# Performance work log

Measured on AMD Instinct MI355X. Metric: run time of the kernel, lower is better.

Reference implementation:

```python
import jax, jax.numpy as jnp
import numpy as np

B = 128        # graphs
N_PER = 1024   # nodes per graph
K = 7          # knn neighbors
X_SIZE = 16
POS_SIZE = 3
H1, H2 = 64, 128
N = B * N_PER
EPS = 1e-5


def _lin_init(key, din, dout):
    kw, kb = jax.random.split(key)
    s = 1.0 / np.sqrt(din)
    w = jax.random.uniform(kw, (din, dout), jnp.float32, -s, s)
    b = jax.random.uniform(kb, (dout,), jnp.float32, -s, s)
    return w, b


def setup_inputs() -> dict:
    key = jax.random.key(0)
    ks = jax.random.split(key, 12)
    x = jax.random.normal(ks[0], (N, X_SIZE), jnp.float32)
    pos = jax.random.normal(ks[1], (N, POS_SIZE), jnp.float32)
    batch = jnp.repeat(jnp.arange(B, dtype=jnp.int32), N_PER)
    wk1, bk1 = _lin_init(ks[2], X_SIZE, H1)
    wq1, bq1 = _lin_init(ks[3], X_SIZE, H1)
    wv1, bv1 = _lin_init(ks[4], X_SIZE, H1)
    ws1, bs1 = _lin_init(ks[5], X_SIZE, H1)
    wk2, bk2 = _lin_init(ks[6], H1, H2)
    wq2, bq2 = _lin_init(ks[7], H1, H2)
    wv2, bv2 = _lin_init(ks[8], H1, H2)
    ws2, bs2 = _lin_init(ks[9], H1, H2)
    g1 = jnp.ones((H1,), jnp.float32); be1 = jnp.zeros((H1,), jnp.float32)
    g2 = jnp.ones((H2,), jnp.float32); be2 = jnp.zeros((H2,), jnp.float32)
    return dict(x=x, pos=pos, batch=batch,
                wk1=wk1, bk1=bk1, wq1=wq1, bq1=bq1, wv1=wv1, bv1=bv1, ws1=ws1, bs1=bs1, g1=g1, be1=be1,
                wk2=wk2, bk2=bk2, wq2=wq2, bq2=bq2, wv2=wv2, bv2=bv2, ws2=ws2, bs2=bs2, g2=g2, be2=be2)


def knn_edges(pos):
    # batch-aware kNN: graphs are equal-sized contiguous blocks of N_PER nodes
    p = pos.reshape(B, N_PER, POS_SIZE)
    def per_graph(pg):
        d = jnp.sum((pg[:, None, :] - pg[None, :, :]) ** 2, axis=-1)  # [n, n]
        d = jnp.where(jnp.eye(N_PER, dtype=bool), jnp.inf, d)          # no self loops
        _, idx = jax.lax.top_k(-d, K)                                   # [n, K]
        return idx
    idx = jax.vmap(per_graph)(p)                       # [B, N_PER, K]
    offs = (jnp.arange(B) * N_PER)[:, None, None]
    src = (idx + offs).reshape(-1)                     # neighbor j (source)
    dst = jnp.broadcast_to(jnp.arange(N_PER)[None, :, None] + offs, (B, N_PER, K)).reshape(-1)
    return src, dst


def res_gated_conv(x, src, dst, wk, bk, wq, bq, wv, bv, ws, bs):
    # out_i = skip(x_i) + sum_{j->i} sigmoid(K x_i + Q x_j) * V x_j
    kf = x @ wk + bk
    qf = x @ wq + bq
    vf = x @ wv + bv
    msg = jax.nn.sigmoid(kf[dst] + qf[src]) * vf[src]  # [E, out]
    agg = jnp.zeros_like(kf).at[dst].add(msg)
    return agg + x @ ws + bs


def batch_norm(x, gamma, beta):
    m = x.mean(0)
    v = jnp.mean((x - m) ** 2, 0)  # biased var (training-mode BN)
    return (x - m) * jax.lax.rsqrt(v + EPS) * gamma + beta


def reference(x, pos, batch, wk1, bk1, wq1, bq1, wv1, bv1, ws1, bs1, g1, be1,
              wk2, bk2, wq2, bq2, wv2, bv2, ws2, bs2, g2, be2):
    src, dst = knn_edges(pos)
    h = jax.nn.relu(batch_norm(res_gated_conv(x, src, dst, wk1, bk1, wq1, bq1, wv1, bv1, ws1, bs1), g1, be1))
    h = jax.nn.relu(batch_norm(res_gated_conv(h, src, dst, wk2, bk2, wq2, bq2, wv2, bv2, ws2, bs2), g2, be2))
    s = jax.ops.segment_sum(h, batch, num_segments=B)
    cnt = jax.ops.segment_sum(jnp.ones((h.shape[0], 1), h.dtype), batch, num_segments=B)
    return s / cnt
```

## Files before the change

kernel.cpp:

```cpp
#include <hip/hip_runtime.h>
#include <hip/hip_bf16.h>

#define BGR   128
#define NPER  1024
#define NK    7
#define NNODES (BGR*NPER)

typedef __attribute__((ext_vector_type(8))) short short8;
typedef __attribute__((ext_vector_type(8))) unsigned short ushort8;
typedef __attribute__((ext_vector_type(4))) float floatx4;

static __device__ __forceinline__ float bf2f(unsigned short u) {
    unsigned int x = ((unsigned int)u) << 16;
    return __builtin_bit_cast(float, x);
}
static __device__ __forceinline__ unsigned short f2bf(float f) {
    unsigned int x = __builtin_bit_cast(unsigned int, f);
    unsigned int lsb = (x >> 16) & 1u;
    x += 0x7fffu + lsb;
    return (unsigned short)(x >> 16);
}
static __device__ __forceinline__ float packdi(float d, int j) {
    unsigned int ub = (__builtin_bit_cast(unsigned int, d) & 0xFFFFFC00u) | (unsigned int)j;
    return __builtin_bit_cast(float, ub);
}

__global__ __launch_bounds__(256) void knn_kernel(const float* __restrict__ pos,
                                                  int* __restrict__ idx) {
    __shared__ __align__(16) floatx4 sp[8 * 129];
    int g     = blockIdx.x >> 4;
    int qbase = (blockIdx.x & 15) << 6;
    int base  = g * NPER;
    const float* pg = pos + (size_t)base * 3;
    for (int t = threadIdx.x; t < NPER * 3; t += 256) {
        float v = pg[t];
        int j = t / 3, comp = t - j * 3;
        int slot = (j >> 7) * 129 + (j & 127);
        ((float*)&sp[slot])[comp] = v;
    }
    __syncthreads();
    for (int j = threadIdx.x; j < NPER; j += 256) {
        int slot = (j >> 7) * 129 + (j & 127);
        floatx4 q = sp[slot];
        sp[slot].w = fmaf(q.x, q.x, fmaf(q.y, q.y, q.z * q.z));
    }
    __syncthreads();

    int lane = threadIdx.x & 63;
    int wv   = (int)threadIdx.x >> 6;
    int grp  = lane >> 3;
    int e    = lane & 7;
    int qA_l = qbase + (wv * 8 + grp) * 2;
    int qB_l = qA_l + 1;
    floatx4 meA = sp[(qA_l >> 7) * 129 + (qA_l & 127)];
    floatx4 meB = sp[(qB_l >> 7) * 129 + (qB_l & 127)];
    float mAx = -2.f * meA.x, mAy = -2.f * meA.y, mAz = -2.f * meA.z;
    float mBx = -2.f * meB.x, mBy = -2.f * meB.y, mBz = -2.f * meB.z;
    const floatx4* cp = sp + e * 129;
    int jbase = e << 7;

    float a0=3e38f,a1=3e38f,a2=3e38f,a3=3e38f,a4=3e38f,a5=3e38f,a6=3e38f,a7=3e38f;
    float c0=3e38f,c1=3e38f,c2=3e38f,c3=3e38f,c4=3e38f,c5=3e38f,c6=3e38f,c7=3e38f;
    for (int jp = 0; jp < 128; jp += 4) {
        #pragma unroll
        for (int u = 0; u < 4; ++u) {
            floatx4 q = cp[jp + u];
            float dA = fmaf(mAx, q.x, fmaf(mAy, q.y, fmaf(mAz, q.z, q.w)));
            float dB = fmaf(mBx, q.x, fmaf(mBy, q.y, fmaf(mBz, q.z, q.w)));
            float tA = packdi(dA, jbase + jp + u);
            float tB = packdi(dB, jbase + jp + u);
            float nA7 = __builtin_amdgcn_fmed3f(a6, a7, tA);
            float nA6 = __builtin_amdgcn_fmed3f(a5, a6, tA);
            float nA5 = __builtin_amdgcn_fmed3f(a4, a5, tA);
            float nA4 = __builtin_amdgcn_fmed3f(a3, a4, tA);
            float nA3 = __builtin_amdgcn_fmed3f(a2, a3, tA);
            float nA2 = __builtin_amdgcn_fmed3f(a1, a2, tA);
            float nA1 = __builtin_amdgcn_fmed3f(a0, a1, tA);
            a0 = fminf(a0, tA);
            a1 = nA1; a2 = nA2; a3 = nA3; a4 = nA4; a5 = nA5; a6 = nA6; a7 = nA7;
            float nB7 = __builtin_amdgcn_fmed3f(c6, c7, tB);
            float nB6 = __builtin_amdgcn_fmed3f(c5, c6, tB);
            float nB5 = __builtin_amdgcn_fmed3f(c4, c5, tB);
            float nB4 = __builtin_amdgcn_fmed3f(c3, c4, tB);
            float nB3 = __builtin_amdgcn_fmed3f(c2, c3, tB);
            float nB2 = __builtin_amdgcn_fmed3f(c1, c2, tB);
            float nB1 = __builtin_amdgcn_fmed3f(c0, c1, tB);
            c0 = fminf(c0, tB);
            c1 = nB1; c2 = nB2; c3 = nB3; c4 = nB4; c5 = nB5; c6 = nB6; c7 = nB7;
        }
    }

    float A[8] = {a0,a1,a2,a3,a4,a5,a6,a7};
    float C[8] = {c0,c1,c2,c3,c4,c5,c6,c7};
    #pragma unroll
    for (int st = 0; st < 2; ++st) {
        int mask = 1 << st;
        #pragma unroll
        for (int ch = 0; ch < 2; ++ch) {
            float* L = ch ? C : A;
            float B[8], T[8];
            #pragma unroll
            for (int i = 0; i < 8; ++i) B[i] = __shfl_xor(L[i], mask);
            #pragma unroll
            for (int i = 0; i < 8; ++i) T[i] = fminf(L[i], B[7 - i]);
            #define CEx(x,y) { float mn = fminf(T[x], T[y]); float mx = fmaxf(T[x], T[y]); T[x] = mn; T[y] = mx; }
            CEx(0,4) CEx(1,5) CEx(2,6) CEx(3,7)
            CEx(0,2) CEx(1,3) CEx(4,6) CEx(5,7)
            CEx(0,1) CEx(2,3) CEx(4,5) CEx(6,7)
            #undef CEx
            #pragma unroll
            for (int i = 0; i < 8; ++i) L[i] = T[i];
        }
    }
    float OA[8], OC[8];
    #pragma unroll
    for (int i = 0; i < 8; ++i) { OA[i] = __shfl_xor(A[i], 4); OC[i] = __shfl_xor(C[i], 4); }

    if (e < 2) {
        float *M, *O;
        int qm_l;
        if (e == 0) { M = A;  O = OA; qm_l = qA_l; }
        else        { M = C;  O = OC; qm_l = qB_l; }
        bool selfInM = (qm_l >> 9) == 0;
        int r[7];
        #pragma unroll
        for (int i = 0; i < 7; ++i) {
            float mm = selfInM ? fminf(M[i + 1], O[6 - i]) : fminf(O[i + 1], M[6 - i]);
            r[i] = base + (int)(__builtin_bit_cast(unsigned int, mm) & 1023u);
        }
        int4* op = (int4*)(idx + (size_t)(base + qm_l) * 8);
        int4 r0, r1;
        r0.x = r[0]; r0.y = r[1]; r0.z = r[2]; r0.w = r[3];
        r1.x = r[4]; r1.y = r[5]; r1.z = r[6]; r1.w = base;
        op[0] = r0;
        op[1] = r1;
    }
}

__global__ __launch_bounds__(256) void feat1_kernel(
    const float* __restrict__ x,
    const float* __restrict__ wk, const float* __restrict__ bk,
    const float* __restrict__ wq, const float* __restrict__ bq,
    const float* __restrict__ wv, const float* __restrict__ bv,
    const float* __restrict__ wsm, const float* __restrict__ bs,
    unsigned int* __restrict__ qv, unsigned int* __restrict__ ks) {
    int c = threadIdx.x & 63;
    float Wk[16], Wq[16], Wv[16], Ws[16];
    #pragma unroll
    for (int k = 0; k < 16; ++k) {
        Wk[k] = wk[k*64+c]; Wq[k] = wq[k*64+c]; Wv[k] = wv[k*64+c]; Ws[k] = wsm[k*64+c];
    }
    float Bk = bk[c], Bq = bq[c], Bv = bv[c], Bs = bs[c];
    int wave = blockIdx.x * (blockDim.x >> 6) + (threadIdx.x >> 6);
    int nw   = gridDim.x * (blockDim.x >> 6);
    for (int n = wave; n < NNODES; n += nw) {
        const float* xr = x + (size_t)n * 16;
        float ak = Bk, aq = Bq, av = Bv, as = Bs;
        #pragma unroll
        for (int k = 0; k < 16; ++k) {
            float xv = xr[k];
            ak += xv * Wk[k]; aq += xv * Wq[k]; av += xv * Wv[k]; as += xv * Ws[k];
        }
        size_t o = (size_t)n * 64 + c;
        qv[o] = ((unsigned int)f2bf(av) << 16) | f2bf(aq);
        ks[o] = ((unsigned int)f2bf(as) << 16) | f2bf(ak);
    }
}

template<int C>
__global__ __launch_bounds__(256) void conv_kernel(
    const unsigned int* __restrict__ qv, const unsigned int* __restrict__ ks,
    const int* __restrict__ idx, unsigned short* __restrict__ h,
    float* __restrict__ part) {
    const int NPB = 256 / C;
    int c   = threadIdx.x & (C - 1);
    int sub = __builtin_amdgcn_readfirstlane((int)(threadIdx.x / C));
    int b     = blockIdx.x;
    int xcd   = b & 7;
    int chunk = b >> 3;
    int graph = xcd * 16 + (chunk >> 5);
    int nblk  = chunk & 31;
    int n0 = graph * NPER + nblk * 32;
    float s = 0.f, s2 = 0.f;
    #pragma unroll 4
    for (int i = sub; i < 32; i += NPB) {
        int n = n0 + i;
        const int4* nb4 = (const int4*)(idx + (size_t)n * 8);
        int4 na = nb4[0];
        int4 nbv = nb4[1];
        unsigned int ku = ks[(size_t)n * C + c];
        float kv  = bf2f((unsigned short)(ku & 0xFFFF));
        float acc = bf2f((unsigned short)(ku >> 16));
        int jj[7] = {na.x, na.y, na.z, na.w, nbv.x, nbv.y, nbv.z};
        #pragma unroll
        for (int k = 0; k < NK; ++k) {
            int j = __builtin_amdgcn_readfirstlane(jj[k]);
            const unsigned int* p = qv + (size_t)j * C;
            unsigned int u = p[c];
            float qvv = bf2f((unsigned short)(u & 0xFFFF));
            float vvv = bf2f((unsigned short)(u >> 16));
            float t = kv + qvv;
            float sg = __builtin_amdgcn_rcpf(1.f + __expf(-t));
            acc = fmaf(sg, vvv, acc);
        }
        unsigned short hb = f2bf(acc);
        h[(size_t)n * C + c] = hb;
        float hv = bf2f(hb);
        s += hv; s2 += hv * hv;
    }
    __shared__ float ls[256], ls2[256];
    ls[threadIdx.x] = s; ls2[threadIdx.x] = s2;
    __syncthreads();
    if (threadIdx.x < C) {
        #pragma unroll
        for (int l = 1; l < NPB; ++l) { s += ls[threadIdx.x + l*C]; s2 += ls2[threadIdx.x + l*C]; }
        part[(size_t)blockIdx.x * 2 * C + threadIdx.x]     = s;
        part[(size_t)blockIdx.x * 2 * C + C + threadIdx.x] = s2;
    }
}

template<int C>
static __device__ __forceinline__ void bnfin_body(
    const float* __restrict__ part, const float* __restrict__ gamma,
    const float* __restrict__ beta, float* __restrict__ ss,
    int c, float* ls, float* ls2) {
    float s = 0.f, s2 = 0.f;
    for (int b = threadIdx.x; b < 4096; b += 256) {
        s  += part[(size_t)b * 2 * C + c];
        s2 += part[(size_t)b * 2 * C + C + c];
    }
    ls[threadIdx.x] = s; ls2[threadIdx.x] = s2;
    __syncthreads();
    for (int st = 128; st > 0; st >>= 1) {
        if (threadIdx.x < st) { ls[threadIdx.x] += ls[threadIdx.x+st]; ls2[threadIdx.x] += ls2[threadIdx.x+st]; }
        __syncthreads();
    }
    if (threadIdx.x == 0) {
        float m   = ls[0] / (float)NNODES;
        float var = ls2[0] / (float)NNODES - m * m;
        float inv = rsqrtf(var + 1e-5f);
        float sc  = gamma[c] * inv;
        ss[c]     = sc;
        ss[C + c] = beta[c] - m * sc;
    }
}

template<int C>
__global__ __launch_bounds__(256) void bnfin_kernel(
    const float* __restrict__ part, const float* __restrict__ gamma,
    const float* __restrict__ beta, float* __restrict__ ss) {
    __shared__ float ls[256], ls2[256];
    bnfin_body<C>(part, gamma, beta, ss, blockIdx.x, ls, ls2);
}

__global__ __launch_bounds__(256) void fin1_wfrag_kernel(
    const float* __restrict__ part, const float* __restrict__ gamma,
    const float* __restrict__ beta, float* __restrict__ ss,
    const float* __restrict__ w0, const float* __restrict__ w1,
    const float* __restrict__ w2, const float* __restrict__ w3,
    unsigned short* __restrict__ frag) {
    __shared__ float ls[256], ls2[256];
    if (blockIdx.x < 64) {
        bnfin_body<64>(part, gamma, beta, ss, blockIdx.x, ls, ls2);
        return;
    }
    int s  = blockIdx.x - 64;
    if (threadIdx.x >= 64) return;
    int m  = s >> 4;
    int kt = (s >> 3) & 1;
    int ct = s & 7;
    const float* w = (m == 0) ? w0 : (m == 1) ? w1 : (m == 2) ? w2 : w3;
    int l = threadIdx.x;
    int col = ct * 16 + (l & 15);
    int kbase = kt * 32 + (l >> 4) * 8;
    unsigned short* out = frag + ((size_t)s * 64 + l) * 8;
    #pragma unroll
    for (int e = 0; e < 8; ++e) out[e] = f2bf(w[(size_t)(kbase + e) * 128 + col]);
}

__global__ __launch_bounds__(256) void feat2_kernel(
    const unsigned short* __restrict__ h1n, const unsigned short* __restrict__ frag,
    const float* __restrict__ ss1,
    const float* __restrict__ b0, const float* __restrict__ b1,
    const float* __restrict__ b2, const float* __restrict__ b3,
    unsigned int* __restrict__ qv2, unsigned int* __restrict__ ks2) {
    __shared__ unsigned short xh[2][2][16][17];
    int m  = threadIdx.x >> 6;
    int l  = threadIdx.x & 63;
    const float* bm = (m == 0) ? b0 : (m == 1) ? b1 : (m == 2) ? b2 : b3;
    int lr = l & 15;
    int gq = l >> 4;
    short8 W0[8], W1[8];
    #pragma unroll
    for (int ct = 0; ct < 8; ++ct) {
        W0[ct] = *(const short8*)(frag + ((size_t)(m * 16 + ct)     * 64 + l) * 8);
        W1[ct] = *(const short8*)(frag + ((size_t)(m * 16 + 8 + ct) * 64 + l) * 8);
    }
    float bvv[8];
    #pragma unroll
    for (int ct = 0; ct < 8; ++ct) bvv[ct] = bm[ct * 16 + lr];

    for (int t = 0; t < 8; ++t) {
        int nt = blockIdx.x * 8 + t;
        int n  = nt * 16 + lr;
        const unsigned short* ar = h1n + (size_t)n * 64 + gq * 8;
        short8 a0r = *(const short8*)ar;
        short8 a1r = *(const short8*)(ar + 32);
        short8 a0, a1;
        #pragma unroll
        for (int e = 0; e < 8; ++e) {
            int c0 = gq * 8 + e;
            float f0 = bf2f((unsigned short)a0r[e]) * ss1[c0] + ss1[64 + c0];
            a0[e] = (short)f2bf(fmaxf(f0, 0.f));
            int c1 = 32 + gq * 8 + e;
            float f1 = bf2f((unsigned short)a1r[e]) * ss1[c1] + ss1[64 + c1];
            a1[e] = (short)f2bf(fmaxf(f1, 0.f));
        }
        #pragma unroll
        for (int ct = 0; ct < 8; ++ct) {
            float bv = bvv[ct];
            floatx4 acc = {bv, bv, bv, bv};
            acc = __builtin_amdgcn_mfma_f32_16x16x32_bf16(a0, W0[ct], acc, 0, 0, 0);
            acc = __builtin_amdgcn_mfma_f32_16x16x32_bf16(a1, W1[ct], acc, 0, 0, 0);
            if (m >= 2) {
                #pragma unroll
                for (int r = 0; r < 4; ++r)
                    xh[ct & 1][m - 2][gq * 4 + r][lr] = f2bf(acc[r]);
            }
            __syncthreads();
            if (m < 2) {
                unsigned int* od = (m == 1) ? qv2 : ks2;
                int set = (m == 1) ? 0 : 1;
                #pragma unroll
                for (int r = 0; r < 4; ++r) {
                    unsigned int lo = f2bf(acc[r]);
                    unsigned int hi = xh[ct & 1][set][gq * 4 + r][lr];
                    od[(size_t)(nt * 16 + gq * 4 + r) * 128 + ct * 16 + lr] = (hi << 16) | lo;
                }
            }
        }
    }
}

__global__ __launch_bounds__(256) void pool_partial_kernel(const unsigned int* __restrict__ h2p,
                                                           const float* __restrict__ ss2,
                                                           float* __restrict__ part) {
    int g = blockIdx.x >> 3;
    int q = blockIdx.x & 7;
    int cp = (threadIdx.x & 63) * 2;
    int isub = threadIdx.x >> 6;
    float sc0 = ss2[cp],     sh0 = ss2[128 + cp];
    float sc1 = ss2[cp + 1], sh1 = ss2[128 + cp + 1];
    float acc0 = 0.f, acc1 = 0.f;
    const unsigned int* hp = h2p + ((size_t)g * NPER + q * 128) * 64 + (cp >> 1);
    for (int i = isub; i < 128; i += 4) {
        unsigned int u = hp[(size_t)i * 64];
        acc0 += fmaxf(bf2f((unsigned short)(u & 0xFFFF)) * sc0 + sh0, 0.f);
        acc1 += fmaxf(bf2f((unsigned short)(u >> 16))    * sc1 + sh1, 0.f);
    }
    __shared__ float red0[256], red1[256];
    red0[threadIdx.x] = acc0; red1[threadIdx.x] = acc1;
    __syncthreads();
    if (threadIdx.x < 64) {
        float s0 = acc0, s1 = acc1;
        #pragma unroll
        for (int k = 1; k < 4; ++k) { s0 += red0[threadIdx.x + 64 * k]; s1 += red1[threadIdx.x + 64 * k]; }
        part[(size_t)blockIdx.x * 128 + cp]     = s0;
        part[(size_t)blockIdx.x * 128 + cp + 1] = s1;
    }
}

__global__ void pool_final_kernel(const float* __restrict__ part, float* __restrict__ out) {
    int g = blockIdx.x, c = threadIdx.x;
    float s = 0.f;
    #pragma unroll
    for (int q = 0; q < 8; ++q) s += part[(size_t)(g * 8 + q) * 128 + c];
    out[(size_t)g * 128 + c] = s * (1.f / 1024.f);
}

extern "C" void kernel_launch(void* const* d_in, const int* in_sizes, int n_in,
                              void* d_out, int out_size, void* d_ws, size_t ws_size,
                              hipStream_t stream) {
    const float* x   = (const float*)d_in[0];
    const float* pos = (const float*)d_in[1];
    const float* wk1 = (const float*)d_in[3];
    const float* bk1 = (const float*)d_in[4];
    const float* wq1 = (const float*)d_in[5];
    const float* bq1 = (const float*)d_in[6];
    const float* wv1 = (const float*)d_in[7];
    const float* bv1 = (const float*)d_in[8];
    const float* ws1 = (const float*)d_in[9];
    const float* bs1 = (const float*)d_in[10];
    const float* g1  = (const float*)d_in[11];
    const float* be1 = (const float*)d_in[12];
    const float* wk2 = (const float*)d_in[13];
    const float* bk2 = (const float*)d_in[14];
    const float* wq2 = (const float*)d_in[15];
    const float* bq2 = (const float*)d_in[16];
    const float* wv2 = (const float*)d_in[17];
    const float* bv2 = (const float*)d_in[18];
    const float* ws2 = (const float*)d_in[19];
    const float* bs2 = (const float*)d_in[20];
    const float* g2  = (const float*)d_in[21];
    const float* be2 = (const float*)d_in[22];
    float* out = (float*)d_out;

    const size_t SZ_QV1 = (size_t)NNODES * 64 * 4;
    const size_t SZ_QV2 = (size_t)NNODES * 128 * 4;

    char* ws = (char*)d_ws;
    size_t off = 0;
    auto alloc = [&](size_t b) { size_t o = off; off += (b + 255) & ~(size_t)255; return o; };

    int* idx              = (int*)(ws + alloc((size_t)NNODES * 8 * 4));
    size_t o_region       = alloc(2 * SZ_QV2);
    unsigned int* qv1     = (unsigned int*)(ws + o_region);
    unsigned int* ks1     = (unsigned int*)(ws + o_region + SZ_QV1);
    unsigned int* qv2     = (unsigned int*)(ws + o_region);
    unsigned int* ks2     = (unsigned int*)(ws + o_region + SZ_QV2);
    unsigned short* h1    = (unsigned short*)(ws + alloc((size_t)NNODES * 64 * 2));
    unsigned short* h2    = (unsigned short*)(ws + alloc((size_t)NNODES * 128 * 2));
    unsigned short* frag  = (unsigned short*)(ws + alloc(64 * 64 * 8 * 2));
    float* part           = (float*)(ws + alloc((size_t)4096 * 2 * 128 * 4));
    float* ss1            = (float*)(ws + alloc(2 * 64 * 4));
    float* ss2            = (float*)(ws + alloc(2 * 128 * 4));
    (void)ws_size; (void)in_sizes; (void)n_in; (void)out_size;

    knn_kernel<<<BGR * 16, 256, 0, stream>>>(pos, idx);
    feat1_kernel<<<1024, 256, 0, stream>>>(x, wk1, bk1, wq1, bq1, wv1, bv1, ws1, bs1,
                                           qv1, ks1);
    conv_kernel<64><<<NNODES / 32, 256, 0, stream>>>(qv1, ks1, idx, h1, part);
    fin1_wfrag_kernel<<<128, 256, 0, stream>>>(part, g1, be1, ss1,
                                               wk2, wq2, wv2, ws2, frag);
    feat2_kernel<<<NNODES / 128, 256, 0, stream>>>(h1, frag, ss1, bk2, bq2, bv2, bs2,
                                                   qv2, ks2);
    conv_kernel<128><<<NNODES / 32, 256, 0, stream>>>(qv2, ks2, idx, h2, part);
    bnfin_kernel<128><<<128, 256, 0, stream>>>(part, g2, be2, ss2);
    pool_partial_kernel<<<BGR * 8, 256, 0, stream>>>((const unsigned int*)h2, ss2, part);
    pool_final_kernel<<<BGR, 128, 0, stream>>>(part, out);
}
```

Baseline: 233.7 us.

## Compute layer-1 feature projections with bf16 MFMA and LDS-packed outputs

Rewrites feat1_kernel so each of the four waves in a block computes one projection (K, Q, V, skip) with the 16x16x32 bf16 MFMA, zero-padding the 16-wide input to K=32. V and skip results are staged through a double-buffered shared-memory tile so the K and Q waves can write the packed bf16 pairs into qv and ks. The grid now gives each block 128 nodes. The aim is to replace the scalar fp32 FMA loop with matrix-core work. In exchange, x is rounded to bf16 before the multiply, half of each MFMA is wasted on padding, a __syncthreads runs per column tile, and each store covers only 64 contiguous bytes per row.

```diff
diff --git a/kernel.cpp b/kernel.cpp
--- a/kernel.cpp
+++ b/kernel.cpp
@@ -144,26 +144,66 @@
     const float* __restrict__ wv, const float* __restrict__ bv,
     const float* __restrict__ wsm, const float* __restrict__ bs,
     unsigned int* __restrict__ qv, unsigned int* __restrict__ ks) {
-    int c = threadIdx.x & 63;
-    float Wk[16], Wq[16], Wv[16], Ws[16];
-    #pragma unroll
-    for (int k = 0; k < 16; ++k) {
-        Wk[k] = wk[k*64+c]; Wq[k] = wq[k*64+c]; Wv[k] = wv[k*64+c]; Ws[k] = wsm[k*64+c];
-    }
-    float Bk = bk[c], Bq = bq[c], Bv = bv[c], Bs = bs[c];
-    int wave = blockIdx.x * (blockDim.x >> 6) + (threadIdx.x >> 6);
-    int nw   = gridDim.x * (blockDim.x >> 6);
-    for (int n = wave; n < NNODES; n += nw) {
-        const float* xr = x + (size_t)n * 16;
-        float ak = Bk, aq = Bq, av = Bv, as = Bs;
-        #pragma unroll
-        for (int k = 0; k < 16; ++k) {
-            float xv = xr[k];
-            ak += xv * Wk[k]; aq += xv * Wq[k]; av += xv * Wv[k]; as += xv * Ws[k];
-        }
-        size_t o = (size_t)n * 64 + c;
-        qv[o] = ((unsigned int)f2bf(av) << 16) | f2bf(aq);
-        ks[o] = ((unsigned int)f2bf(as) << 16) | f2bf(ak);
+    __shared__ unsigned short xh[2][2][16][17];
+    int m  = threadIdx.x >> 6;
+    int l  = threadIdx.x & 63;
+    int lr = l & 15;
+    int gq = l >> 4;
+    const float* wm  = (m == 0) ? wk : (m == 1) ? wq : (m == 2) ? wv : wsm;
+    const float* bmp = (m == 0) ? bk : (m == 1) ? bq : (m == 2) ? bv : bs;
+    short8 W[4];
+    #pragma unroll
+    for (int ct = 0; ct < 4; ++ct) {
+        short8 w;
+        #pragma unroll
+        for (int e = 0; e < 8; ++e) {
+            int k = gq * 8 + e;
+            float v = (gq < 2) ? wm[(size_t)k * 64 + ct * 16 + lr] : 0.f;
+            w[e] = (short)f2bf(v);
+        }
+        W[ct] = w;
+    }
+    float bvv[4];
+    #pragma unroll
+    for (int ct = 0; ct < 4; ++ct) bvv[ct] = bmp[ct * 16 + lr];
+
+    for (int t = 0; t < 8; ++t) {
+        int nt = blockIdx.x * 8 + t;
+        int n  = nt * 16 + lr;
+        short8 a;
+        if (gq < 2) {
+            const floatx4* xr = (const floatx4*)(x + (size_t)n * 16 + gq * 8);
+            floatx4 v0 = xr[0], v1 = xr[1];
+            a[0] = (short)f2bf(v0.x); a[1] = (short)f2bf(v0.y);
+            a[2] = (short)f2bf(v0.z); a[3] = (short)f2bf(v0.w);
+            a[4] = (short)f2bf(v1.x); a[5] = (short)f2bf(v1.y);
+            a[6] = (short)f2bf(v1.z); a[7] = (short)f2bf(v1.w);
+        } else {
+            #pragma unroll
+            for (int e = 0; e < 8; ++e) a[e] = 0;
+        }
+        #pragma unroll
+        for (int ct = 0; ct < 4; ++ct) {
+            float bv = bvv[ct];
+            floatx4 acc = {bv, bv, bv, bv};
+            acc = __builtin_amdgcn_mfma_f32_16x16x32_bf16(a, W[ct], acc, 0, 0, 0);
+            if (m >= 2) {
+                #pragma unroll
+                for (int r = 0; r < 4; ++r)
+                    xh[ct & 1][m - 2][gq * 4 + r][lr] = f2bf(acc[r]);
+            }
+            __syncthreads();
+            if (m < 2) {
+                unsigned int* od = (m == 1) ? qv : ks;
+                int set = (m == 1) ? 0 : 1;
+                #pragma unroll
+                for (int r = 0; r < 4; ++r) {
+                    unsigned int lo = f2bf(acc[r]);
+                    unsigned int hi = xh[ct & 1][set][gq * 4 + r][lr];
+                    od[(size_t)(nt * 16 + gq * 4 + r) * 64 + ct * 16 + lr] = (hi << 16) | lo;
+                }
+            }
+        }
     }
 }
 
@@ -427,8 +467,8 @@
     (void)ws_size; (void)in_sizes; (void)n_in; (void)out_size;
 
     knn_kernel<<<BGR * 16, 256, 0, stream>>>(pos, idx);
-    feat1_kernel<<<1024, 256, 0, stream>>>(x, wk1, bk1, wq1, bq1, wv1, bv1, ws1, bs1,
-                                           qv1, ks1);
+    feat1_kernel<<<NNODES / 128, 256, 0, stream>>>(x, wk1, bk1, wq1, bq1, wv1, bv1, ws1, bs1,
+                                                   qv1, ks1);
     conv_kernel<64><<<NNODES / 32, 256, 0, stream>>>(qv1, ks1, idx, h1, part);
     fin1_wfrag_kernel<<<128, 256, 0, stream>>>(part, g1, be1, ss1,
                                                wk2, wq2, wv2, ws2, frag);
```

Measured after the change: 221.7 us. 1.05x faster.
